# Optimization experiments

Measured on AMD Instinct MI355X. Metric: run time of the kernel, lower is better.

Reference implementation:

```python
import jax, jax.numpy as jnp
import numpy as np

B, R, T = 128, 36, 40
E, V, H1, H2, PH, VOC = 1024, 2048, 1024, 1024, 256, 10000


def _lstm_cell(x, h, c, Wi, Wh, b):
    # torch gate order: i, f, g, o
    g = x @ Wi.T + h @ Wh.T + b
    i, f, gg, o = jnp.split(g, 4, axis=-1)
    c_new = jax.nn.sigmoid(f) * c + jax.nn.sigmoid(i) * jnp.tanh(gg)
    h_new = jax.nn.sigmoid(o) * jnp.tanh(c_new)
    return h_new, c_new


def setup_inputs() -> dict:
    key = jax.random.key(0)
    ks = jax.random.split(key, 20)
    s = 0.05
    Vmat = jax.random.normal(ks[0], (B, R, V), jnp.float32)
    enc_features = jax.random.normal(ks[1], (B, V), jnp.float32)
    union_vfeats = jax.random.normal(ks[2], (B, V), jnp.float32)
    captions = jax.random.randint(ks[3], (B, T), 0, VOC, jnp.int32)
    lengths = jax.random.randint(ks[4], (B,), 1, T + 1, jnp.int32)
    lengths = jnp.sort(lengths)[::-1].at[0].set(T)  # sorted descending, max first
    embed_W = jax.random.normal(ks[5], (VOC, E), jnp.float32) * s
    Wi1 = jax.random.normal(ks[6], (4 * H1, H2 + V + E), jnp.float32) * s
    Wh1 = jax.random.normal(ks[7], (4 * H1, H1), jnp.float32) * s
    b1 = jax.random.normal(ks[8], (4 * H1,), jnp.float32) * s
    Wi2 = jax.random.normal(ks[9], (4 * H2, H1 + V), jnp.float32) * s
    Wh2 = jax.random.normal(ks[10], (4 * H2, H2), jnp.float32) * s
    b2 = jax.random.normal(ks[11], (4 * H2,), jnp.float32) * s
    Wva = jax.random.normal(ks[12], (PH, V), jnp.float32) * s
    bva = jax.random.normal(ks[13], (PH,), jnp.float32) * s
    Wha = jax.random.normal(ks[14], (PH, H1), jnp.float32) * s
    bha = jax.random.normal(ks[15], (PH,), jnp.float32) * s
    wa = jax.random.normal(ks[16], (PH,), jnp.float32) * s
    ba = jax.random.normal(ks[17], (), jnp.float32) * s
    Wl = jax.random.normal(ks[18], (VOC, H2), jnp.float32) * s
    bl = jax.random.normal(ks[19], (VOC,), jnp.float32) * s
    return dict(Vmat=Vmat, enc_features=enc_features, union_vfeats=union_vfeats,
                captions=captions, lengths=lengths, embed_W=embed_W,
                Wi1=Wi1, Wh1=Wh1, b1=b1, Wi2=Wi2, Wh2=Wh2, b2=b2,
                Wva=Wva, bva=bva, Wha=Wha, bha=bha, wa=wa, ba=ba, Wl=Wl, bl=bl)


def reference(Vmat, enc_features, union_vfeats, captions, lengths, embed_W,
              Wi1, Wh1, b1, Wi2, Wh2, b2, Wva, bva, Wha, bha, wa, ba, Wl, bl):
    embeddings = embed_W[captions]                      # [B, T, E]
    Va = Vmat @ Wva.T + bva                             # [B, R, PH] (precompute, step-invariant)

    def step(carry, xs):
        h1, c1, h2, c2 = carry
        emb_t, i = xs
        active = (lengths > i)[:, None]                 # [B, 1]
        x1 = jnp.concatenate([h2, union_vfeats, emb_t], axis=-1)
        h1n, c1n = _lstm_cell(x1, h1, c1, Wi1, Wh1, b1)
        # top-down attention over R regions
        logit = jnp.tanh(Va + (h1n @ Wha.T + bha)[:, None, :]) @ wa + ba  # [B, R]
        atten = jax.nn.softmax(logit, axis=1)
        av = jnp.einsum('br,brd->bd', atten, Vmat)      # [B, V]
        x2 = jnp.concatenate([av, h1n], axis=-1)
        h2n, c2n = _lstm_cell(x2, h2, c2, Wi2, Wh2, b2)
        logits = h2n @ Wl.T + bl                        # [B, VOC]
        # state freeze + zero outputs for finished sequences (ragged masking)
        h1 = jnp.where(active, h1n, h1); c1 = jnp.where(active, c1n, c1)
        h2 = jnp.where(active, h2n, h2); c2 = jnp.where(active, c2n, c2)
        out_t = jnp.where(active, logits, 0.0)
        return (h1, c1, h2, c2), out_t

    z1 = jnp.zeros((B, H1), jnp.float32)
    z2 = jnp.zeros((B, H2), jnp.float32)
    xs = (jnp.transpose(embeddings, (1, 0, 2)), jnp.arange(T, dtype=jnp.int32))
    _, outs = jax.lax.scan(step, (z1, z1, z2, z2), xs)  # [T, B, VOC]
    return jnp.transpose(outs, (1, 0, 2))               # [B, T, VOC]
```

## Files before the change

kernel.cpp:

```cpp
#include <hip/hip_runtime.h>

#define EPI_PART 0
#define EPI_BF16D 1

#define T_ 40
#define VOC_ 10000

typedef __attribute__((ext_vector_type(8))) short bf16x8;
typedef __attribute__((ext_vector_type(4))) short short4v;
typedef __attribute__((ext_vector_type(8))) short short8v;
typedef __attribute__((ext_vector_type(4))) float float4v;
typedef __attribute__((ext_vector_type(4))) float f32x4;

__device__ __forceinline__ float bf2f(short s) {
  unsigned u = ((unsigned)(unsigned short)s) << 16;
  float f; __builtin_memcpy(&f, &u, 4); return f;
}
__device__ __forceinline__ short f2bf(float f) {
  unsigned u; __builtin_memcpy(&u, &f, 4);
  u += 0x7FFFu + ((u >> 16) & 1u);
  return (short)(u >> 16);
}
__device__ __forceinline__ float sigm(float x) { return 1.f / (1.f + expf(-x)); }

__device__ __forceinline__ size_t pkidx(int row, int k, int K) {
  return (size_t)(row >> 4) * 16 * K + (size_t)(k >> 3) * 128 + (size_t)((row & 15) * 8 + (k & 7));
}


__global__ __launch_bounds__(256) void k_f2bf_split(const float* __restrict__ s,
    short* __restrict__ dh, short* __restrict__ dl, long n4) {
  long i = (long)blockIdx.x * 256 + threadIdx.x;
  long stride = (long)gridDim.x * 256;
  for (; i < n4; i += stride) {
    float4v f = ((const float4v*)s)[i];
    short4v oh, ol;
    #pragma unroll
    for (int j = 0; j < 4; j++) {
      short h = f2bf(f[j]); oh[j] = h; ol[j] = f2bf(f[j] - bf2f(h));
    }
    ((short4v*)dh)[i] = oh;
    ((short4v*)dl)[i] = ol;
  }
}

__global__ __launch_bounds__(256) void k_permpk(short* __restrict__ dh, short* __restrict__ dl,
    const float* __restrict__ s1, int ld1, int col0, int K1,
    const float* __restrict__ s2, int ld2, int Ktot) {
  int K4 = Ktot >> 2;
  long n4 = 4096L * K4;
  long stride = (long)gridDim.x * 256;
  for (long i = (long)blockIdx.x * 256 + threadIdx.x; i < n4; i += stride) {
    int p = (int)(i / K4);
    int c = ((int)(i % K4)) << 2;
    int orig = ((p & 3) << 10) + (p >> 2);
    const float* src = (c < K1) ? (s1 + (long)orig * ld1 + col0 + c)
                                : (s2 + (long)orig * ld2 + (c - K1));
    float4v f = *(const float4v*)src;
    short4v oh, ol;
    #pragma unroll
    for (int j = 0; j < 4; j++) {
      short h = f2bf(f[j]); oh[j] = h; ol[j] = f2bf(f[j] - bf2f(h));
    }
    size_t d = pkidx(p, c, Ktot);
    *(short4v*)&dh[d] = oh;
    if (dl) *(short4v*)&dl[d] = ol;
  }
}

__global__ __launch_bounds__(256) void k_packpk(short* __restrict__ dh, short* __restrict__ dl,
    const float* __restrict__ src, int ld, int Nr, int Nsrc, int K) {
  int K4 = K >> 2;
  long n4 = (long)Nr * K4;
  long stride = (long)gridDim.x * 256;
  for (long i = (long)blockIdx.x * 256 + threadIdx.x; i < n4; i += stride) {
    int row = (int)(i / K4);
    int c = ((int)(i % K4)) << 2;
    float4v f = {0.f, 0.f, 0.f, 0.f};
    if (row < Nsrc) f = *(const float4v*)(src + (long)row * ld + c);
    short4v oh, ol;
    #pragma unroll
    for (int j = 0; j < 4; j++) {
      short h = f2bf(f[j]); oh[j] = h; ol[j] = f2bf(f[j] - bf2f(h));
    }
    size_t d = pkidx(row, c, K);
    *(short4v*)&dh[d] = oh;
    if (dl) *(short4v*)&dl[d] = ol;
  }
}

__global__ __launch_bounds__(256) void k_perm_bias(float* __restrict__ d1, const float* __restrict__ s1,
                                                   float* __restrict__ d2, const float* __restrict__ s2) {
  int p = blockIdx.x * 256 + threadIdx.x;
  if (p < 4096) {
    int orig = ((p & 3) << 10) + (p >> 2);
    d1[p] = s1[orig];
    d2[p] = s2[orig];
  }
}

__global__ __launch_bounds__(256) void k_gather_emb(short* __restrict__ dst, const float* __restrict__ embW,
                                                    const int* __restrict__ cap) {
  int i = blockIdx.x * 256 + threadIdx.x;
  if (i >= 5120 * 128) return;
  int row = i >> 7, c8 = (i & 127) << 3;
  int tok = cap[row];
  const float4v* s = (const float4v*)(embW + (long)tok * 1024 + c8);
  float4v f0 = s[0], f1 = s[1];
  short8v o;
  #pragma unroll
  for (int j = 0; j < 4; j++) { o[j] = f2bf(f0[j]); o[4 + j] = f2bf(f1[j]); }
  *(short8v*)(dst + (long)row * 1024 + c8) = o;
}

__global__ __launch_bounds__(256) void k_pack_whaf(float* __restrict__ dst, const float* __restrict__ Wha) {
  int i = blockIdx.x * 256 + threadIdx.x;
  int hb = i >> 8, ph = i & 255;
  float4v a = *(const float4v*)(Wha + (long)ph * 1024 + hb * 8);
  float4v b4 = *(const float4v*)(Wha + (long)ph * 1024 + hb * 8 + 4);
  *(float4v*)(dst + ((long)hb * 256 + ph) * 8) = a;
  *(float4v*)(dst + ((long)hb * 256 + ph) * 8 + 4) = b4;
}


template<int NCS, bool SA, bool SW, int EPI>
__device__ __forceinline__ void gemm_body(short* sh, int bx, int ks, int mb,
    const short* __restrict__ A, const short* __restrict__ Alo, int lda,
    const short* __restrict__ W, const short* __restrict__ Wlo, int K,
    int Npad, int Mtot, float* __restrict__ part, short* __restrict__ outbf) {
  const int tid = threadIdx.x;
  const int l = tid & 63, w = tid >> 6;
  const int rif = l & 15, kg = l >> 4;
  const int n0 = bx * 128;
  const int k0 = ks * NCS * 64;
  const int mbase = mb * 128;

  f32x4 acc[8][2];
  #pragma unroll
  for (int m = 0; m < 8; m++) {
    acc[m][0] = (f32x4){0.f, 0.f, 0.f, 0.f};
    acc[m][1] = (f32x4){0.f, 0.f, 0.f, 0.f};
  }

  bf16x8 wh[2][2][2], wl[2][2][2];
  size_t wt0 = (size_t)(n0 / 16 + w * 2) * 16 * K + (size_t)l * 8;
  size_t wt1 = wt0 + (size_t)16 * K;
  auto loadW = [&](int c, int slot) {
    size_t base = (size_t)((k0 + c * 64) >> 3) * 128;
    #pragma unroll
    for (int sk = 0; sk < 2; sk++) {
      wh[slot][sk][0] = *(const bf16x8*)(W + wt0 + base + sk * 512);
      wh[slot][sk][1] = *(const bf16x8*)(W + wt1 + base + sk * 512);
      if (SW) {
        wl[slot][sk][0] = *(const bf16x8*)(Wlo + wt0 + base + sk * 512);
        wl[slot][sk][1] = *(const bf16x8*)(Wlo + wt1 + base + sk * 512);
      }
    }
  };

  short8v rA[4], rL[4];
  const int srow = tid >> 3;
  const int scol = (tid & 7) * 8;
  auto ldA = [&](int c) {
    #pragma unroll
    for (int j = 0; j < 4; j++) {
      size_t g = (size_t)(mbase + j * 32 + srow) * lda + k0 + c * 64 + scol;
      rA[j] = *(const short8v*)(A + g);
      if (SA) rL[j] = *(const short8v*)(Alo + g);
    }
  };
  auto stA = [&]() {
    #pragma unroll
    for (int j = 0; j < 4; j++) {
      int row = j * 32 + srow;
      int idx = row * 64 + (scol ^ ((row & 7) << 3));
      *(short8v*)&sh[idx] = rA[j];
      if (SA) *(short8v*)&sh[8192 + idx] = rL[j];
    }
  };
  auto compute = [&](int slot) {
    #pragma unroll
    for (int sk = 0; sk < 2; sk++) {
      int colb = ((sk * 32 + kg * 8) ^ ((rif & 7) << 3));
      #pragma unroll
      for (int m = 0; m < 8; m++) {
        int idx = (m * 16 + rif) * 64 + colb;
        bf16x8 ah = *(const bf16x8*)&sh[idx];
        bf16x8 al;
        if (SA) al = *(const bf16x8*)&sh[8192 + idx];
        #pragma unroll
        for (int nf = 0; nf < 2; nf++) {
          acc[m][nf] = __builtin_amdgcn_mfma_f32_16x16x32_bf16(ah, wh[slot][0][nf] * 0 + wh[slot][sk][nf], acc[m][nf], 0, 0, 0);
          if (SA) acc[m][nf] = __builtin_amdgcn_mfma_f32_16x16x32_bf16(al, wh[slot][sk][nf], acc[m][nf], 0, 0, 0);
          if (SW) acc[m][nf] = __builtin_amdgcn_mfma_f32_16x16x32_bf16(ah, wl[slot][sk][nf], acc[m][nf], 0, 0, 0);
        }
      }
    }
  };

  ldA(0); loadW(0, 0);
  stA();
  __syncthreads();
  #pragma unroll
  for (int c = 0; c < NCS; c++) {
    if (c + 1 < NCS) { ldA(c + 1); loadW(c + 1, (c + 1) & 1); }
    compute(c & 1);
    __syncthreads();
    if (c + 1 < NCS) { stA(); __syncthreads(); }
  }

  #pragma unroll
  for (int nf = 0; nf < 2; nf++) {
    int colw = n0 + (w * 2 + nf) * 16 + rif;
    #pragma unroll
    for (int m = 0; m < 8; m++) {
      #pragma unroll
      for (int j = 0; j < 4; j++) {
        int row = m * 16 + kg * 4 + j;
        if constexpr (EPI == EPI_PART) {
          part[((size_t)ks * Mtot + mbase + row) * Npad + colw] = acc[m][nf][j];
        } else {
          outbf[(size_t)(mbase + row) * Npad + colw] = f2bf(acc[m][nf][j]);
        }
      }
    }
  }
}

template<int NCS, bool SA, bool SW, int EPI>
__global__ __launch_bounds__(256) void k_g6(
    const short* __restrict__ A, const short* __restrict__ Alo, int lda,
    const short* __restrict__ W, const short* __restrict__ Wlo, int K,
    int Npad, int Mtot, float* __restrict__ part, short* __restrict__ outbf) {
  __shared__ short sh[SA ? 16384 : 8192];
  gemm_body<NCS, SA, SW, EPI>(sh, blockIdx.x, blockIdx.y, blockIdx.z,
      A, Alo, lda, W, Wlo, K, Npad, Mtot, part, outbf);
}

__global__ __launch_bounds__(256) void k_sum(const float* __restrict__ part,
    float* __restrict__ out, const float* __restrict__ bias,
    long n4, int N4, int KS, long stride4) {
  long i = (long)blockIdx.x * 256 + threadIdx.x;
  if (i >= n4) return;
  float4v a = *(const float4v*)&bias[(i % N4) * 4];
  for (int s = 0; s < KS; s++) {
    float4v p = ((const float4v*)part)[s * stride4 + i];
    #pragma unroll
    for (int j = 0; j < 4; j++) a[j] += p[j];
  }
  ((float4v*)out)[i] = a;
}

__global__ __launch_bounds__(256) void k_epi2(
    const float* __restrict__ part, const float* __restrict__ b2p,
    float* __restrict__ cstate,
    const short* __restrict__ xcur_hi, const short* __restrict__ xcur_lo,
    short* __restrict__ xnext_hi, short* __restrict__ xnext_lo,
    short* __restrict__ h2n_hi, short* __restrict__ h2n_lo,
    const int* __restrict__ lengths, int t) {
  int i = blockIdx.x * 256 + threadIdx.x;
  int b = i >> 10, h = i & 1023;
  float4v g = *(const float4v*)&b2p[h * 4];
  #pragma unroll
  for (int s = 0; s < 8; s++) {
    float4v p = *(const float4v*)&part[((size_t)s * 128 + b) * 4096 + h * 4];
    #pragma unroll
    for (int j = 0; j < 4; j++) g[j] += p[j];
  }
  float co = cstate[b * 1024 + h];
  float cn = sigm(g[1]) * co + sigm(g[0]) * tanhf(g[2]);
  float hn = sigm(g[3]) * tanhf(cn);
  bool act = lengths[b] > t;
  cstate[b * 1024 + h] = act ? cn : co;
  short hi16 = f2bf(hn);
  short lo16 = f2bf(hn - bf2f(hi16));
  h2n_hi[b * 1024 + h] = hi16;
  h2n_lo[b * 1024 + h] = lo16;
  short oh = xcur_hi[b * 2048 + h];
  short ol = xcur_lo[b * 2048 + h];
  xnext_hi[b * 2048 + h] = act ? hi16 : oh;
  xnext_lo[b * 2048 + h] = act ? lo16 : ol;
}

__global__ __launch_bounds__(256) void k_dualA(
    const short* __restrict__ xcH, const short* __restrict__ xcL,
    const short* __restrict__ W1dHi, const short* __restrict__ W1dLo,
    float* __restrict__ partA,
    const short* __restrict__ h2nHi, const short* __restrict__ h2nLo,
    const short* __restrict__ WlPK, float* __restrict__ partLG, int t) {
  __shared__ short sh[16384];
  int bx = blockIdx.x;
  if (bx < 256) {
    if (t >= T_) return;
    gemm_body<4, true, true, EPI_PART>(sh, bx & 31, bx >> 5, 0,
        xcH, xcL, 2048, W1dHi, W1dLo, 2048, 4096, 128, partA, nullptr);
  } else {
    if (t == 0) return;
    int f = bx - 256;
    gemm_body<8, true, false, EPI_PART>(sh, f % 79, f / 79, 0,
        h2nHi, h2nLo, 1024, WlPK, nullptr, 1024, 10112, 128, partLG, nullptr);
  }
}

__global__ __launch_bounds__(256) void k_dualB(
    const float* __restrict__ partA,
    const float* __restrict__ zuv, const short* __restrict__ zemb,
    float* __restrict__ c1,
    const short* __restrict__ xcH, const short* __restrict__ xcL,
    short* __restrict__ xnH, short* __restrict__ xnL,
    short* __restrict__ x2H, short* __restrict__ x2L,
    const float* __restrict__ WhaF, const float* __restrict__ bha,
    const float* __restrict__ wa, const float* __restrict__ ba,
    const float* __restrict__ Va, const float* __restrict__ Vmat,
    const int* __restrict__ lengths,
    const float* __restrict__ partLG, const float* __restrict__ bl,
    float* __restrict__ out, int t) {
  __shared__ float h1f[1024];
  __shared__ float ha_sh[256];
  __shared__ float wa_sh[256];
  __shared__ float logit_sh[40];
  __shared__ float p_sh[40];
  const int tid = threadIdx.x;
  if (blockIdx.x >= 128) {
    if (t == 0) return;
    int id = (blockIdx.x - 128) * 256 + tid;
    if (id >= 320000) return;
    int b = id / 2500, q = (id % 2500) * 4;
    bool act = lengths[b] > (t - 1);
    float4v a = {0.f, 0.f, 0.f, 0.f};
    if (act) {
      a = *(const float4v*)&bl[q];
      #pragma unroll
      for (int s = 0; s < 2; s++) {
        float4v p = *(const float4v*)&partLG[((size_t)s * 128 + b) * 10112 + q];
        #pragma unroll
        for (int j = 0; j < 4; j++) a[j] += p[j];
      }
    }
    *(float4v*)&out[((size_t)b * T_ + (t - 1)) * VOC_ + q] = a;
    return;
  }
  if (t >= T_) return;
  const int b = blockIdx.x;
  const bool act = lengths[b] > t;
  #pragma unroll
  for (int i = 0; i < 4; i++) {
    int h = i * 256 + tid;
    float4v g = {0.f, 0.f, 0.f, 0.f};
    #pragma unroll
    for (int s = 0; s < 8; s++) {
      float4v p = *(const float4v*)&partA[((size_t)s * 128 + b) * 4096 + h * 4];
      #pragma unroll
      for (int j = 0; j < 4; j++) g[j] += p[j];
    }
    float4v z = *(const float4v*)&zuv[(size_t)b * 4096 + h * 4];
    short4v e4 = *(const short4v*)&zemb[((size_t)b * T_ + t) * 4096 + h * 4];
    #pragma unroll
    for (int j = 0; j < 4; j++) g[j] += z[j] + bf2f(e4[j]);
    float co = c1[b * 1024 + h];
    float cn = sigm(g[1]) * co + sigm(g[0]) * tanhf(g[2]);
    float hn = sigm(g[3]) * tanhf(cn);
    c1[b * 1024 + h] = act ? cn : co;
    h1f[h] = hn;
    short hi16 = f2bf(hn);
    short lo16 = f2bf(hn - bf2f(hi16));
    x2H[b * 4096 + 2048 + h] = hi16;
    x2L[b * 4096 + 2048 + h] = lo16;
    short oh = xcH[b * 2048 + 1024 + h];
    short ol = xcL[b * 2048 + 1024 + h];
    xnH[b * 2048 + 1024 + h] = act ? hi16 : oh;
    xnL[b * 2048 + 1024 + h] = act ? lo16 : ol;
    x2H[b * 4096 + 3072 + h] = xcH[b * 2048 + h];
    x2L[b * 4096 + 3072 + h] = xcL[b * 2048 + h];
  }
  wa_sh[tid] = wa[tid];
  __syncthreads();
  {
    float a = 0.f;
    const float* wp = WhaF + tid * 8;
    #pragma unroll 4
    for (int hb = 0; hb < 128; hb++) {
      float4v w0 = *(const float4v*)(wp + (size_t)hb * 2048);
      float4v w1 = *(const float4v*)(wp + (size_t)hb * 2048 + 4);
      #pragma unroll
      for (int j = 0; j < 4; j++) a += w0[j] * h1f[hb * 8 + j] + w1[j] * h1f[hb * 8 + 4 + j];
    }
    ha_sh[tid] = a + bha[tid];
  }
  __syncthreads();
  {
    const int r0 = tid >> 3, sl = tid & 7;
    const float ba0 = ba[0];
    for (int r = r0; r < 36; r += 32) {
      const float4v* va4 = (const float4v*)(Va + ((long)b * 36 + r) * 256 + sl * 32);
      float part = 0.f;
      #pragma unroll
      for (int q = 0; q < 8; q++) {
        float4v v4 = va4[q];
        #pragma unroll
        for (int j = 0; j < 4; j++) {
          int ph = sl * 32 + q * 4 + j;
          part += tanhf(v4[j] + ha_sh[ph]) * wa_sh[ph];
        }
      }
      part += __shfl_down(part, 4, 8);
      part += __shfl_down(part, 2, 8);
      part += __shfl_down(part, 1, 8);
      if (sl == 0) logit_sh[r] = part + ba0;
    }
  }
  __syncthreads();
  if (tid < 64) {
    float v = (tid < 36) ? logit_sh[tid] : -3.4e38f;
    float m = v;
    #pragma unroll
    for (int off = 32; off > 0; off >>= 1) m = fmaxf(m, __shfl_xor(m, off));
    float e = (tid < 36) ? expf(v - m) : 0.f;
    float s = e;
    #pragma unroll
    for (int off = 32; off > 0; off >>= 1) s += __shfl_xor(s, off);
    if (tid < 36) p_sh[tid] = e / s;
  }
  __syncthreads();
  {
    float av[8];
    #pragma unroll
    for (int j = 0; j < 8; j++) av[j] = 0.f;
    const float* vb = Vmat + (long)b * (36 * 2048) + tid * 8;
    for (int r = 0; r < 36; r++) {
      float p = p_sh[r];
      float4v v0 = *(const float4v*)(vb + (long)r * 2048);
      float4v v1 = *(const float4v*)(vb + (long)r * 2048 + 4);
      #pragma unroll
      for (int j = 0; j < 4; j++) { av[j] += p * v0[j]; av[4 + j] += p * v1[j]; }
    }
    short8v oh, ol;
    #pragma unroll
    for (int j = 0; j < 8; j++) {
      short h = f2bf(av[j]);
      oh[j] = h;
      ol[j] = f2bf(av[j] - bf2f(h));
    }
    *(short8v*)(x2H + b * 4096 + tid * 8) = oh;
    *(short8v*)(x2L + b * 4096 + tid * 8) = ol;
  }
}

extern "C" void kernel_launch(void* const* d_in, const int* in_sizes, int n_in,
                              void* d_out, int out_size, void* d_ws, size_t ws_size,
                              hipStream_t stream) {
  const float* Vmat = (const float*)d_in[0];
  const float* uv   = (const float*)d_in[2];
  const int* captions = (const int*)d_in[3];
  const int* lengths  = (const int*)d_in[4];
  const float* embW = (const float*)d_in[5];
  const float* Wi1 = (const float*)d_in[6];
  const float* Wh1 = (const float*)d_in[7];
  const float* b1  = (const float*)d_in[8];
  const float* Wi2 = (const float*)d_in[9];
  const float* Wh2 = (const float*)d_in[10];
  const float* b2  = (const float*)d_in[11];
  const float* Wva = (const float*)d_in[12];
  const float* bva = (const float*)d_in[13];
  const float* Wha = (const float*)d_in[14];
  const float* bha = (const float*)d_in[15];
  const float* wa  = (const float*)d_in[16];
  const float* ba  = (const float*)d_in[17];
  const float* Wl  = (const float*)d_in[18];
  const float* bl  = (const float*)d_in[19];
  (void)in_sizes; (void)n_in; (void)out_size; (void)ws_size;

  char* ws = (char*)d_ws;
  size_t off = 0;
  auto alloc = [&](size_t bytes) { void* p = ws + off; off += (bytes + 255) & ~255UL; return p; };
  short* W1dHi = (short*)alloc(4096L * 2048 * 2);
  short* W1dLo = (short*)alloc(4096L * 2048 * 2);
  short* W2dHi = (short*)alloc(4096L * 4096 * 2);
  short* W2dLo = (short*)alloc(4096L * 4096 * 2);
  short* WlPK  = (short*)alloc(10112L * 1024 * 2);
  float* WhaF  = (float*)alloc(128L * 256 * 8 * 4);
  float* VaBuf = (float*)alloc(4608L * 256 * 4);
  float* Z1uvB = (float*)alloc(128L * 4096 * 4);
  short* Z1embB = (short*)alloc(5120L * 4096 * 2);
  float* partA = (float*)alloc(8L * 128 * 4096 * 4);
  float* partLG = (float*)alloc(2L * 128 * 10112 * 4);
  float* b1P = (float*)alloc(4096 * 4);
  float* b2P = (float*)alloc(4096 * 4);
  short* x1Hi = (short*)alloc(2L * 128 * 2048 * 2);
  short* x1Lo = (short*)alloc(2L * 128 * 2048 * 2);
  short* x2Hi = (short*)alloc(128L * 4096 * 2);
  short* x2Lo = (short*)alloc(128L * 4096 * 2);
  short* h2nHi = (short*)alloc(128L * 1024 * 2);
  short* h2nLo = (short*)alloc(128L * 1024 * 2);
  float* c1 = (float*)alloc(128L * 1024 * 4);
  float* c2 = (float*)alloc(128L * 1024 * 4);

  short* W1uvHi = W2dHi;
  short* W1uvLo = W2dHi + 4096L * 2048;
  float* zuvPart = (float*)(W2dHi + 4096L * 4096);
  short* uvHi = W2dHi + 4096L * 4096 + 4096L * 2048 + 2097152;
  short* uvLo = uvHi + 128L * 2048;
  short* WvaHi = uvLo + 128L * 2048;
  short* WvaLo = WvaHi + 256L * 2048;
  float* vaPart = (float*)W2dHi;
  short* W1ePk = (short*)partA;
  short* AembBF = (short*)partA + 4096L * 1024;
  short* VmatHi = Z1embB;
  short* VmatLo = Z1embB + 4608L * 2048;

  (void)hipMemsetAsync(x1Hi, 0, 2L * 128 * 2048 * 2, stream);
  (void)hipMemsetAsync(x1Lo, 0, 2L * 128 * 2048 * 2, stream);
  (void)hipMemsetAsync(c1, 0, 128L * 1024 * 4, stream);
  (void)hipMemsetAsync(c2, 0, 128L * 1024 * 4, stream);

  k_packpk<<<2048, 256, 0, stream>>>(WlPK, nullptr, Wl, 1024, 10112, 10000, 1024);
  k_pack_whaf<<<128, 256, 0, stream>>>(WhaF, Wha);
  k_packpk<<<512, 256, 0, stream>>>(WvaHi, WvaLo, Wva, 2048, 256, 256, 2048);
  k_permpk<<<2048, 256, 0, stream>>>(W1dHi, W1dLo, Wi1, 4096, 0, 1024, Wh1, 1024, 2048);
  k_permpk<<<2048, 256, 0, stream>>>(W1uvHi, W1uvLo, Wi1, 4096, 1024, 2048, Wi1, 4096, 2048);
  k_permpk<<<1024, 256, 0, stream>>>(W1ePk, nullptr, Wi1, 4096, 3072, 1024, Wi1, 4096, 1024);
  k_perm_bias<<<16, 256, 0, stream>>>(b1P, b1, b2P, b2);
  k_gather_emb<<<2560, 256, 0, stream>>>(AembBF, embW, captions);
  k_f2bf_split<<<2048, 256, 0, stream>>>(Vmat, VmatHi, VmatLo, 128L * 36 * 2048 / 4);
  k_f2bf_split<<<64, 256, 0, stream>>>(uv, uvHi, uvLo, 128L * 2048 / 4);

  k_g6<4, true, true, EPI_PART><<<dim3(32, 8, 1), 256, 0, stream>>>(
      uvHi, uvLo, 2048, W1uvHi, W1uvLo, 2048, 4096, 128, zuvPart, nullptr);
  k_sum<<<512, 256, 0, stream>>>(zuvPart, Z1uvB, b1P, 131072, 1024, 8, 131072);
  k_g6<4, true, true, EPI_PART><<<dim3(2, 8, 36), 256, 0, stream>>>(
      VmatHi, VmatLo, 2048, WvaHi, WvaLo, 2048, 256, 4608, vaPart, nullptr);
  k_sum<<<1152, 256, 0, stream>>>(vaPart, VaBuf, bva, 294912, 64, 8, 294912);
  k_permpk<<<4096, 256, 0, stream>>>(W2dHi, W2dLo, Wi2, 3072, 0, 3072, Wh2, 1024, 4096);
  k_g6<16, false, false, EPI_BF16D><<<dim3(32, 1, 40), 256, 0, stream>>>(
      AembBF, nullptr, 1024, W1ePk, nullptr, 1024, 4096, 5120, nullptr, Z1embB);

  for (int t = 0; t <= T_; t++) {
    const short* xcH = x1Hi + (size_t)(t & 1) * (128 * 2048);
    const short* xcL = x1Lo + (size_t)(t & 1) * (128 * 2048);
    short* xnH = x1Hi + (size_t)((t + 1) & 1) * (128 * 2048);
    short* xnL = x1Lo + (size_t)((t + 1) & 1) * (128 * 2048);
    k_dualA<<<414, 256, 0, stream>>>(xcH, xcL, W1dHi, W1dLo, partA,
        h2nHi, h2nLo, WlPK, partLG, t);
    k_dualB<<<1378, 256, 0, stream>>>(partA, Z1uvB, Z1embB, c1,
        xcH, xcL, xnH, xnL, x2Hi, x2Lo, WhaF, bha, wa, ba, VaBuf, Vmat,
        lengths, partLG, bl, (float*)d_out, t);
    if (t < T_) {
      k_g6<8, true, true, EPI_PART><<<dim3(32, 8, 1), 256, 0, stream>>>(
          x2Hi, x2Lo, 4096, W2dHi, W2dLo, 4096, 4096, 128, partA, nullptr);
      k_epi2<<<512, 256, 0, stream>>>(partA, b2P, c2,
          xcH, xcL, xnH, xnL, h2nHi, h2nLo, lengths, t);
    }
  }
}
```

Before: 3.689 ms.

## Fuse logits epilogue into GEMM, halve split-K, batch attention four rows per block

The output-projection GEMM now applies bias, the active-sequence mask and the store to the output tensor directly in its epilogue. This removes the partial-logit buffer and the separate reduction blocks. The first LSTM's gate GEMM uses 4 K-splits instead of 8, which halves the partial-sum traffic. Attention is moved into its own kernel that handles 4 batch rows per block, so the Wha weight stream is reused across rows. In exchange, far fewer workgroups run (79 logit blocks without split-K, 32 attention blocks), so each step may lose parallelism and become more latency-bound.

Result: slower. 6.085 ms (+64.9%).

```diff
diff --git a/kernel.cpp b/kernel.cpp
--- a/kernel.cpp
+++ b/kernel.cpp
@@ -2,6 +2,7 @@
 
 #define EPI_PART 0
 #define EPI_BF16D 1
+#define EPI_LOGITS 2
 
 #define T_ 40
 #define VOC_ 10000
@@ -127,7 +128,9 @@
 __device__ __forceinline__ void gemm_body(short* sh, int bx, int ks, int mb,
     const short* __restrict__ A, const short* __restrict__ Alo, int lda,
     const short* __restrict__ W, const short* __restrict__ Wlo, int K,
-    int Npad, int Mtot, float* __restrict__ part, short* __restrict__ outbf) {
+    int Npad, int Mtot, float* __restrict__ part, short* __restrict__ outbf,
+    const int* __restrict__ lengths, int tt, const float* __restrict__ blg,
+    float* __restrict__ outlog) {
   const int tid = threadIdx.x;
   const int l = tid & 63, w = tid >> 6;
   const int rif = l & 15, kg = l >> 4;
@@ -190,7 +193,7 @@
         if (SA) al = *(const bf16x8*)&sh[8192 + idx];
         #pragma unroll
         for (int nf = 0; nf < 2; nf++) {
-          acc[m][nf] = __builtin_amdgcn_mfma_f32_16x16x32_bf16(ah, wh[slot][0][nf] * 0 + wh[slot][sk][nf], acc[m][nf], 0, 0, 0);
+          acc[m][nf] = __builtin_amdgcn_mfma_f32_16x16x32_bf16(ah, wh[slot][sk][nf], acc[m][nf], 0, 0, 0);
           if (SA) acc[m][nf] = __builtin_amdgcn_mfma_f32_16x16x32_bf16(al, wh[slot][sk][nf], acc[m][nf], 0, 0, 0);
           if (SW) acc[m][nf] = __builtin_amdgcn_mfma_f32_16x16x32_bf16(ah, wl[slot][sk][nf], acc[m][nf], 0, 0, 0);
         }
@@ -219,8 +222,14 @@
         int row = m * 16 + kg * 4 + j;
         if constexpr (EPI == EPI_PART) {
           part[((size_t)ks * Mtot + mbase + row) * Npad + colw] = acc[m][nf][j];
+        } else if constexpr (EPI == EPI_BF16D) {
+          outbf[(size_t)(mbase + row) * Npad + colw] = f2bf(acc[m][nf][j]);
         } else {
-          outbf[(size_t)(mbase + row) * Npad + colw] = f2bf(acc[m][nf][j]);
+          if (colw < VOC_) {
+            bool act = lengths[row] > tt;
+            outlog[((size_t)row * T_ + tt) * VOC_ + colw] =
+                act ? (acc[m][nf][j] + blg[colw]) : 0.f;
+          }
         }
       }
     }
@@ -234,7 +243,7 @@
     int Npad, int Mtot, float* __restrict__ part, short* __restrict__ outbf) {
   __shared__ short sh[SA ? 16384 : 8192];
   gemm_body<NCS, SA, SW, EPI>(sh, blockIdx.x, blockIdx.y, blockIdx.z,
-      A, Alo, lda, W, Wlo, K, Npad, Mtot, part, outbf);
+      A, Alo, lda, W, Wlo, K, Npad, Mtot, part, outbf, nullptr, 0, nullptr, nullptr);
 }
 
 __global__ __launch_bounds__(256) void k_sum(const float* __restrict__ part,
@@ -287,22 +296,26 @@
     const short* __restrict__ W1dHi, const short* __restrict__ W1dLo,
     float* __restrict__ partA,
     const short* __restrict__ h2nHi, const short* __restrict__ h2nLo,
-    const short* __restrict__ WlPK, float* __restrict__ partLG, int t) {
+    const short* __restrict__ WlPK,
+    const int* __restrict__ lengths, const float* __restrict__ bl,
+    float* __restrict__ out, int t) {
   __shared__ short sh[16384];
   int bx = blockIdx.x;
-  if (bx < 256) {
+  if (bx < 128) {
     if (t >= T_) return;
-    gemm_body<4, true, true, EPI_PART>(sh, bx & 31, bx >> 5, 0,
-        xcH, xcL, 2048, W1dHi, W1dLo, 2048, 4096, 128, partA, nullptr);
+    gemm_body<8, true, true, EPI_PART>(sh, bx & 31, bx >> 5, 0,
+        xcH, xcL, 2048, W1dHi, W1dLo, 2048, 4096, 128, partA, nullptr,
+        nullptr, 0, nullptr, nullptr);
   } else {
     if (t == 0) return;
-    int f = bx - 256;
-    gemm_body<8, true, false, EPI_PART>(sh, f % 79, f / 79, 0,
-        h2nHi, h2nLo, 1024, WlPK, nullptr, 1024, 10112, 128, partLG, nullptr);
-  }
-}
-
-__global__ __launch_bounds__(256) void k_dualB(
+    int f = bx - 128;
+    gemm_body<16, true, false, EPI_LOGITS>(sh, f, 0, 0,
+        h2nHi, h2nLo, 1024, WlPK, nullptr, 1024, 10112, 128, nullptr, nullptr,
+        lengths, t - 1, bl, out);
+  }
+}
+
+__global__ __launch_bounds__(256) void k_attn4(
     const float* __restrict__ partA,
     const float* __restrict__ zuv, const short* __restrict__ zemb,
     float* __restrict__ c1,
@@ -312,123 +325,121 @@
     const float* __restrict__ WhaF, const float* __restrict__ bha,
     const float* __restrict__ wa, const float* __restrict__ ba,
     const float* __restrict__ Va, const float* __restrict__ Vmat,
-    const int* __restrict__ lengths,
-    const float* __restrict__ partLG, const float* __restrict__ bl,
-    float* __restrict__ out, int t) {
-  __shared__ float h1f[1024];
-  __shared__ float ha_sh[256];
+    const int* __restrict__ lengths, int t) {
+  __shared__ float h1f[4096];
+  __shared__ float ha_sh[1024];
   __shared__ float wa_sh[256];
-  __shared__ float logit_sh[40];
-  __shared__ float p_sh[40];
+  __shared__ float logit_sh[160];
+  __shared__ float p_sh[160];
   const int tid = threadIdx.x;
-  if (blockIdx.x >= 128) {
-    if (t == 0) return;
-    int id = (blockIdx.x - 128) * 256 + tid;
-    if (id >= 320000) return;
-    int b = id / 2500, q = (id % 2500) * 4;
-    bool act = lengths[b] > (t - 1);
-    float4v a = {0.f, 0.f, 0.f, 0.f};
-    if (act) {
-      a = *(const float4v*)&bl[q];
+  const int b0 = blockIdx.x * 4;
+
+  #pragma unroll
+  for (int bq = 0; bq < 4; bq++) {
+    const int b = b0 + bq;
+    const bool act = lengths[b] > t;
+    #pragma unroll
+    for (int i = 0; i < 4; i++) {
+      int h = i * 256 + tid;
+      float4v g = {0.f, 0.f, 0.f, 0.f};
       #pragma unroll
-      for (int s = 0; s < 2; s++) {
-        float4v p = *(const float4v*)&partLG[((size_t)s * 128 + b) * 10112 + q];
+      for (int s = 0; s < 4; s++) {
+        float4v p = *(const float4v*)&partA[((size_t)s * 128 + b) * 4096 + h * 4];
         #pragma unroll
-        for (int j = 0; j < 4; j++) a[j] += p[j];
+        for (int j = 0; j < 4; j++) g[j] += p[j];
       }
-    }
-    *(float4v*)&out[((size_t)b * T_ + (t - 1)) * VOC_ + q] = a;
-    return;
-  }
-  if (t >= T_) return;
-  const int b = blockIdx.x;
-  const bool act = lengths[b] > t;
-  #pragma unroll
-  for (int i = 0; i < 4; i++) {
-    int h = i * 256 + tid;
-    float4v g = {0.f, 0.f, 0.f, 0.f};
-    #pragma unroll
-    for (int s = 0; s < 8; s++) {
-      float4v p = *(const float4v*)&partA[((size_t)s * 128 + b) * 4096 + h * 4];
+      float4v z = *(const float4v*)&zuv[(size_t)b * 4096 + h * 4];
+      short4v e4 = *(const short4v*)&zemb[((size_t)b * T_ + t) * 4096 + h * 4];
       #pragma unroll
-      for (int j = 0; j < 4; j++) g[j] += p[j];
-    }
-    float4v z = *(const float4v*)&zuv[(size_t)b * 4096 + h * 4];
-    short4v e4 = *(const short4v*)&zemb[((size_t)b * T_ + t) * 4096 + h * 4];
-    #pragma unroll
-    for (int j = 0; j < 4; j++) g[j] += z[j] + bf2f(e4[j]);
-    float co = c1[b * 1024 + h];
-    float cn = sigm(g[1]) * co + sigm(g[0]) * tanhf(g[2]);
-    float hn = sigm(g[3]) * tanhf(cn);
-    c1[b * 1024 + h] = act ? cn : co;
-    h1f[h] = hn;
-    short hi16 = f2bf(hn);
-    short lo16 = f2bf(hn - bf2f(hi16));
-    x2H[b * 4096 + 2048 + h] = hi16;
-    x2L[b * 4096 + 2048 + h] = lo16;
-    short oh = xcH[b * 2048 + 1024 + h];
-    short ol = xcL[b * 2048 + 1024 + h];
-    xnH[b * 2048 + 1024 + h] = act ? hi16 : oh;
-    xnL[b * 2048 + 1024 + h] = act ? lo16 : ol;
-    x2H[b * 4096 + 3072 + h] = xcH[b * 2048 + h];
-    x2L[b * 4096 + 3072 + h] = xcL[b * 2048 + h];
+      for (int j = 0; j < 4; j++) g[j] += z[j] + bf2f(e4[j]);
+      float co = c1[b * 1024 + h];
+      float cn = sigm(g[1]) * co + sigm(g[0]) * tanhf(g[2]);
+      float hn = sigm(g[3]) * tanhf(cn);
+      c1[b * 1024 + h] = act ? cn : co;
+      h1f[bq * 1024 + h] = hn;
+      short hi16 = f2bf(hn);
+      short lo16 = f2bf(hn - bf2f(hi16));
+      x2H[b * 4096 + 2048 + h] = hi16;
+      x2L[b * 4096 + 2048 + h] = lo16;
+      short oh = xcH[b * 2048 + 1024 + h];
+      short ol = xcL[b * 2048 + 1024 + h];
+      xnH[b * 2048 + 1024 + h] = act ? hi16 : oh;
+      xnL[b * 2048 + 1024 + h] = act ? lo16 : ol;
+      x2H[b * 4096 + 3072 + h] = xcH[b * 2048 + h];
+      x2L[b * 4096 + 3072 + h] = xcL[b * 2048 + h];
+    }
   }
   wa_sh[tid] = wa[tid];
   __syncthreads();
   {
-    float a = 0.f;
+    float a0 = 0.f, a1 = 0.f, a2 = 0.f, a3 = 0.f;
     const float* wp = WhaF + tid * 8;
-    #pragma unroll 4
+    #pragma unroll 2
     for (int hb = 0; hb < 128; hb++) {
       float4v w0 = *(const float4v*)(wp + (size_t)hb * 2048);
       float4v w1 = *(const float4v*)(wp + (size_t)hb * 2048 + 4);
       #pragma unroll
-      for (int j = 0; j < 4; j++) a += w0[j] * h1f[hb * 8 + j] + w1[j] * h1f[hb * 8 + 4 + j];
-    }
-    ha_sh[tid] = a + bha[tid];
+      for (int j = 0; j < 4; j++) {
+        a0 += w0[j] * h1f[hb * 8 + j] + w1[j] * h1f[hb * 8 + 4 + j];
+        a1 += w0[j] * h1f[1024 + hb * 8 + j] + w1[j] * h1f[1024 + hb * 8 + 4 + j];
+        a2 += w0[j] * h1f[2048 + hb * 8 + j] + w1[j] * h1f[2048 + hb * 8 + 4 + j];
+        a3 += w0[j] * h1f[3072 + hb * 8 + j] + w1[j] * h1f[3072 + hb * 8 + 4 + j];
+      }
+    }
+    float bh = bha[tid];
+    ha_sh[tid] = a0 + bh;
+    ha_sh[256 + tid] = a1 + bh;
+    ha_sh[512 + tid] = a2 + bh;
+    ha_sh[768 + tid] = a3 + bh;
   }
   __syncthreads();
   {
     const int r0 = tid >> 3, sl = tid & 7;
     const float ba0 = ba[0];
-    for (int r = r0; r < 36; r += 32) {
-      const float4v* va4 = (const float4v*)(Va + ((long)b * 36 + r) * 256 + sl * 32);
-      float part = 0.f;
-      #pragma unroll
-      for (int q = 0; q < 8; q++) {
-        float4v v4 = va4[q];
+    #pragma unroll
+    for (int bq = 0; bq < 4; bq++) {
+      for (int r = r0; r < 36; r += 32) {
+        const float4v* va4 = (const float4v*)(Va + ((long)(b0 + bq) * 36 + r) * 256 + sl * 32);
+        float part = 0.f;
         #pragma unroll
-        for (int j = 0; j < 4; j++) {
-          int ph = sl * 32 + q * 4 + j;
-          part += tanhf(v4[j] + ha_sh[ph]) * wa_sh[ph];
+        for (int q = 0; q < 8; q++) {
+          float4v v4 = va4[q];
+          #pragma unroll
+          for (int j = 0; j < 4; j++) {
+            int ph = sl * 32 + q * 4 + j;
+            part += tanhf(v4[j] + ha_sh[bq * 256 + ph]) * wa_sh[ph];
+          }
         }
+        part += __shfl_down(part, 4, 8);
+        part += __shfl_down(part, 2, 8);
+        part += __shfl_down(part, 1, 8);
+        if (sl == 0) logit_sh[bq * 40 + r] = part + ba0;
       }
-      part += __shfl_down(part, 4, 8);
-      part += __shfl_down(part, 2, 8);
-      part += __shfl_down(part, 1, 8);
-      if (sl == 0) logit_sh[r] = part + ba0;
-    }
-  }
-  __syncthreads();
-  if (tid < 64) {
-    float v = (tid < 36) ? logit_sh[tid] : -3.4e38f;
-    float m = v;
-    #pragma unroll
-    for (int off = 32; off > 0; off >>= 1) m = fmaxf(m, __shfl_xor(m, off));
-    float e = (tid < 36) ? expf(v - m) : 0.f;
-    float s = e;
-    #pragma unroll
-    for (int off = 32; off > 0; off >>= 1) s += __shfl_xor(s, off);
-    if (tid < 36) p_sh[tid] = e / s;
+    }
   }
   __syncthreads();
   {
+    int wv = tid >> 6, ln = tid & 63;
+    float v = (ln < 36) ? logit_sh[wv * 40 + ln] : -3.4e38f;
+    float m = v;
+    #pragma unroll
+    for (int o = 32; o > 0; o >>= 1) m = fmaxf(m, __shfl_xor(m, o));
+    float e = (ln < 36) ? expf(v - m) : 0.f;
+    float s = e;
+    #pragma unroll
+    for (int o = 32; o > 0; o >>= 1) s += __shfl_xor(s, o);
+    if (ln < 36) p_sh[wv * 40 + ln] = e / s;
+  }
+  __syncthreads();
+  #pragma unroll
+  for (int bq = 0; bq < 4; bq++) {
+    const int b = b0 + bq;
     float av[8];
     #pragma unroll
     for (int j = 0; j < 8; j++) av[j] = 0.f;
     const float* vb = Vmat + (long)b * (36 * 2048) + tid * 8;
     for (int r = 0; r < 36; r++) {
-      float p = p_sh[r];
+      float p = p_sh[bq * 40 + r];
       float4v v0 = *(const float4v*)(vb + (long)r * 2048);
       float4v v1 = *(const float4v*)(vb + (long)r * 2048 + 4);
       #pragma unroll
@@ -482,8 +493,7 @@
   float* VaBuf = (float*)alloc(4608L * 256 * 4);
   float* Z1uvB = (float*)alloc(128L * 4096 * 4);
   short* Z1embB = (short*)alloc(5120L * 4096 * 2);
-  float* partA = (float*)alloc(8L * 128 * 4096 * 4);
-  float* partLG = (float*)alloc(2L * 128 * 10112 * 4);
+  float* partA = (float*)alloc((4096L * 1024 + 5120L * 1024) * 2);
   float* b1P = (float*)alloc(4096 * 4);
   float* b2P = (float*)alloc(4096 * 4);
   short* x1Hi = (short*)alloc(2L * 128 * 2048 * 2);
@@ -539,12 +549,12 @@
     const short* xcL = x1Lo + (size_t)(t & 1) * (128 * 2048);
     short* xnH = x1Hi + (size_t)((t + 1) & 1) * (128 * 2048);
     short* xnL = x1Lo + (size_t)((t + 1) & 1) * (128 * 2048);
-    k_dualA<<<414, 256, 0, stream>>>(xcH, xcL, W1dHi, W1dLo, partA,
-        h2nHi, h2nLo, WlPK, partLG, t);
-    k_dualB<<<1378, 256, 0, stream>>>(partA, Z1uvB, Z1embB, c1,
-        xcH, xcL, xnH, xnL, x2Hi, x2Lo, WhaF, bha, wa, ba, VaBuf, Vmat,
-        lengths, partLG, bl, (float*)d_out, t);
+    k_dualA<<<207, 256, 0, stream>>>(xcH, xcL, W1dHi, W1dLo, partA,
+        h2nHi, h2nLo, WlPK, lengths, bl, (float*)d_out, t);
     if (t < T_) {
+      k_attn4<<<32, 256, 0, stream>>>(partA, Z1uvB, Z1embB, c1,
+          xcH, xcL, xnH, xnL, x2Hi, x2Lo, WhaF, bha, wa, ba, VaBuf, Vmat,
+          lengths, t);
       k_g6<8, true, true, EPI_PART><<<dim3(32, 8, 1), 256, 0, stream>>>(
           x2Hi, x2Lo, 4096, W2dHi, W2dLo, 4096, 4096, 128, partA, nullptr);
       k_epi2<<<512, 256, 0, stream>>>(partA, b2P, c2,
```
